# Kernel tuning notes

Hardware: AMD Instinct MI355X
Metric: run time of the kernel (lower is better)

## Reference

```python
import jax, jax.numpy as jnp
import numpy as np

B, S = 16, 256                     # batch, seq_len
CB, DB = 8, 256                    # control_bits, data_bits
IN_DIM = CB + DB                   # 264
OUT = DB                           # output_bits defaults to data_bits
H = 512                            # hidden_state_dim (LSTM controller)
M = 64                             # memory_content_size
R = 4                              # read heads
N = S                              # memory_addresses_size = -1 -> seq_len
_SPLITS = [R * M, R, M, 1, M, M, R, 1, 1, 3 * R]
XI = int(np.sum(_SPLITS))          # interface vector size = 471
_OFF = np.cumsum(_SPLITS)


def setup_inputs():
    ks = jax.random.split(jax.random.key(0), 6)
    sc = lambda k, shape: jax.random.normal(k, shape, jnp.float32) * 0.02
    return {
        "inputs": jax.random.normal(ks[0], (B, S, IN_DIM), jnp.float32),
        "Wx": sc(ks[1], (IN_DIM + R * M, 4 * H)),
        "Wh": sc(ks[2], (H, 4 * H)),
        "b_lstm": jnp.zeros((4 * H,), jnp.float32),
        "W_xi": sc(ks[3], (H, XI)),
        "b_xi": jnp.zeros((XI,), jnp.float32),
        "W_y": sc(ks[4], (H, OUT)),
        "W_r": sc(ks[5], (R * M, OUT)),
        "b_y": jnp.zeros((OUT,), jnp.float32),
    }


def _oneplus(x):
    return 1.0 + jax.nn.softplus(x)


def _content_weights(mem, keys, beta):
    # mem [B,N,M], keys [B,K,M], beta [B,K] -> softmax over N: [B,K,N]
    mem_n = mem / (jnp.linalg.norm(mem, axis=-1, keepdims=True) + 1e-6)
    key_n = keys / (jnp.linalg.norm(keys, axis=-1, keepdims=True) + 1e-6)
    sim = jnp.einsum('bkm,bnm->bkn', key_n, mem_n)
    return jax.nn.softmax(beta[..., None] * sim, axis=-1)


def _allocation(usage):
    # DNC paper allocation weighting via ascending usage sort
    idx = jnp.argsort(usage, axis=-1)
    u_s = jnp.take_along_axis(usage, idx, axis=-1)
    prod_excl = jnp.concatenate([jnp.ones_like(u_s[:, :1]), jnp.cumprod(u_s, axis=-1)[:, :-1]], axis=-1)
    a_s = (1.0 - u_s) * prod_excl
    inv = jnp.argsort(idx, axis=-1)
    return jnp.take_along_axis(a_s, inv, axis=-1)


def _dnc_forward(inputs, Wx, Wh, b_lstm, W_xi, b_xi, W_y, W_r_out, b_y):
    b = inputs.shape[0]
    eye = jnp.eye(N, dtype=inputs.dtype)

    def step(carry, x):
        h, c, mem, usage, link, prec, w_r, w_w, r_vec = carry
        # LSTM controller on [input, prev read vectors]
        ctrl_in = jnp.concatenate([x, r_vec.reshape(b, R * M)], axis=-1)
        gates = ctrl_in @ Wx + h @ Wh + b_lstm
        i_g, f_g, g_g, o_g = jnp.split(gates, 4, axis=-1)
        c = jax.nn.sigmoid(f_g) * c + jax.nn.sigmoid(i_g) * jnp.tanh(g_g)
        h = jax.nn.sigmoid(o_g) * jnp.tanh(c)

        # interface vector split
        xi = h @ W_xi + b_xi
        k_r = xi[:, :_OFF[0]].reshape(b, R, M)
        beta_r = _oneplus(xi[:, _OFF[0]:_OFF[1]])
        k_w = xi[:, _OFF[1]:_OFF[2]][:, None, :]
        beta_w = _oneplus(xi[:, _OFF[2]:_OFF[3]])
        erase = jax.nn.sigmoid(xi[:, _OFF[3]:_OFF[4]])
        w_vec = xi[:, _OFF[4]:_OFF[5]]
        free = jax.nn.sigmoid(xi[:, _OFF[5]:_OFF[6]])
        g_a = jax.nn.sigmoid(xi[:, _OFF[6]:_OFF[7]])
        g_w = jax.nn.sigmoid(xi[:, _OFF[7]:_OFF[8]])
        pi = jax.nn.softmax(xi[:, _OFF[8]:_OFF[9]].reshape(b, R, 3), axis=-1)

        # usage / allocation (content-free addressing)
        psi = jnp.prod(1.0 - free[:, :, None] * w_r, axis=1)           # [B,N]
        usage = (usage + w_w - usage * w_w) * psi
        alloc = _allocation(usage)

        # write weighting + memory scatter update
        c_w = _content_weights(mem, k_w, beta_w)[:, 0]                 # [B,N]
        w_w = g_w * (g_a * alloc + (1.0 - g_a) * c_w)
        mem = mem * (1.0 - w_w[:, :, None] * erase[:, None, :]) + w_w[:, :, None] * w_vec[:, None, :]

        # temporal linkage
        link = (1.0 - w_w[:, :, None] - w_w[:, None, :]) * link + w_w[:, :, None] * prec[:, None, :]
        link = link * (1.0 - eye)
        prec = (1.0 - jnp.sum(w_w, axis=-1, keepdims=True)) * prec + w_w

        # read weightings (backward / content / forward modes)
        fwd_w = jnp.einsum('bij,brj->bri', link, w_r)
        bwd_w = jnp.einsum('bji,brj->bri', link, w_r)
        c_r = _content_weights(mem, k_r, beta_r)                       # [B,R,N]
        w_r = pi[..., 0:1] * bwd_w + pi[..., 1:2] * c_r + pi[..., 2:3] * fwd_w
        r_vec = jnp.einsum('brn,bnm->brm', w_r, mem)                   # [B,R,M]

        y = h @ W_y + r_vec.reshape(b, R * M) @ W_r_out + b_y
        return (h, c, mem, usage, link, prec, w_r, w_w, r_vec), y

    z = jnp.zeros
    carry0 = (z((b, H)), z((b, H)), z((b, N, M)), z((b, N)), z((b, N, N)),
              z((b, N)), z((b, R, N)), z((b, N)), z((b, R, M)))
    _, ys = jax.lax.scan(step, carry0, jnp.swapaxes(inputs, 0, 1))
    return jnp.swapaxes(ys, 0, 1)                                      # [B,S,OUT]


def reference(inputs, Wx, Wh, b_lstm, W_xi, b_xi, W_y, W_r, b_y):
    return _dnc_forward(inputs, Wx, Wh, b_lstm, W_xi, b_xi, W_y, W_r, b_y)
```

## Files before the change

### kernel.cpp

```cpp
#include <hip/hip_runtime.h>
#include <cstddef>

#define DEV __device__ __forceinline__

constexpr int S_ = 256;
constexpr int NB = 256;
constexpr int NT = 256;


constexpr size_t bH    = 0;
constexpr size_t bC    = 1024;
constexpr size_t bXI   = 1536;
constexpr size_t bKNR  = 2048;
constexpr size_t bALC  = 2304;
constexpr size_t bCW   = 2560;
constexpr size_t bWW   = 2816;
constexpr size_t bNRM  = 3072;
constexpr size_t bUSG  = 3328;
constexpr size_t bRV   = 3584;
constexpr size_t bYH   = 3840;
constexpr size_t bSCL  = 4096;
constexpr size_t bPI   = 4128;
constexpr size_t bERS  = 4160;
constexpr size_t bWVC  = 4224;
constexpr size_t bPRC  = 4288;
constexpr size_t bWR   = 4800;
constexpr size_t bFWD  = 5824;
constexpr size_t bBWDP = 6848;
constexpr size_t bFLG  = 10944;
constexpr size_t bMEM  = 11456;
constexpr size_t bLNK  = 27840;
constexpr size_t bGT   = 93376;
constexpr size_t bGCT  = 95424;
constexpr size_t bSTF  = 95456;
constexpr size_t PB    = 95488;
constexpr size_t WS_TOTAL = PB*16;

typedef unsigned long long u64_;
union F2U { u64_ u; float2 f; };
DEV float2 ld2_agt(const float* p){ F2U c; c.u=__hip_atomic_load((const u64_*)p,__ATOMIC_RELAXED,__HIP_MEMORY_SCOPE_AGENT); return c.f; }
DEV void   st2_agt(float* p, float2 v){ F2U c; c.f=v; __hip_atomic_store((u64_*)p,c.u,__ATOMIC_RELAXED,__HIP_MEMORY_SCOPE_AGENT); }
DEV float  ld_agt(const float* p){ return __hip_atomic_load((float*)p,__ATOMIC_RELAXED,__HIP_MEMORY_SCOPE_AGENT); }
DEV void   st_agt(float* p,float v){ __hip_atomic_store(p,v,__ATOMIC_RELAXED,__HIP_MEMORY_SCOPE_AGENT); }
DEV float  ld_sys(const float* p){ return __hip_atomic_load((float*)p,__ATOMIC_RELAXED,__HIP_MEMORY_SCOPE_SYSTEM); }
DEV void   st_sys(float* p,float v){ __hip_atomic_store(p,v,__ATOMIC_RELAXED,__HIP_MEMORY_SCOPE_SYSTEM); }

DEV float sigm(float x){ return 1.0f/(1.0f+expf(-x)); }
DEV float oneplus_(float x){ float sp = (x>20.0f)? x : log1pf(expf(x)); return 1.0f+sp; }

DEV float wredsum(float v){
  #pragma unroll
  for (int o=32;o>0;o>>=1) v += __shfl_xor(v,o);
  return v;
}
DEV float hredsum32(float v){
  #pragma unroll
  for (int o=16;o>0;o>>=1) v += __shfl_xor(v,o);
  return v;
}
DEV float wredmax(float v){
  #pragma unroll
  for (int o=32;o>0;o>>=1) v = fmaxf(v,__shfl_xor(v,o));
  return v;
}
DEV float bredsum(float v, float* red){
  v = wredsum(v);
  if ((threadIdx.x&63)==0) red[threadIdx.x>>6]=v;
  __syncthreads();
  float r = red[0]+red[1]+red[2]+red[3];
  __syncthreads();
  return r;
}
DEV float bredmax(float v, float* red){
  v = wredmax(v);
  if ((threadIdx.x&63)==0) red[threadIdx.x>>6]=v;
  __syncthreads();
  float r = fmaxf(fmaxf(red[0],red[1]),fmaxf(red[2],red[3]));
  __syncthreads();
  return r;
}

DEV void cbar(float* wsb, unsigned ep, int ci){
  unsigned* flg = (unsigned*)(wsb + bFLG);
  __syncthreads();
  if (threadIdx.x < 64){
    if (threadIdx.x == 0)
      __hip_atomic_store(flg + (size_t)ci*32, ep, __ATOMIC_RELAXED, __HIP_MEMORY_SCOPE_AGENT);
    const int l = threadIdx.x;
    bool ok;
    do {
      unsigned v = (l<16) ? __hip_atomic_load(flg + (size_t)l*32,
                      __ATOMIC_RELAXED, __HIP_MEMORY_SCOPE_AGENT) : ep;
      ok = __all(v >= ep);
      if (!ok) __builtin_amdgcn_s_sleep(1);
    } while (!ok);
  }
  __syncthreads();
}

__global__ void k_zero(float* __restrict__ ws){
  size_t i = (size_t)blockIdx.x*blockDim.x + threadIdx.x;
  size_t st = (size_t)gridDim.x*blockDim.x;
  for (; i<WS_TOTAL; i+=st) ws[i]=0.0f;
}

__global__ __launch_bounds__(NT, 2) void k_dnc(
    const float* __restrict__ xin, const float* __restrict__ Wx,
    const float* __restrict__ Wh,  const float* __restrict__ bl,
    const float* __restrict__ Wxi, const float* __restrict__ bxi,
    const float* __restrict__ Wy,  const float* __restrict__ Wr,
    const float* __restrict__ by,  float* __restrict__ out,
    float* __restrict__ ws)
{
  __shared__ float smem[14336];
  const int tid  = threadIdx.x;
  const int bid  = blockIdx.x;
  const int lane = tid & 63, wv = tid >> 6;
  const int x  = bid & 7;
  const int q  = bid >> 3;
  const int s  = q & 1;
  const int ci = q >> 1;
  const int b  = x + (s<<3);
  float* wsb = ws + (size_t)b*PB;
  const int gb = ci;
  const int gh = s;
  float* wsg = ws + (size_t)gb*PB;
  unsigned ep = 0;

  for (int t=0; t<S_; ++t){
    {
      unsigned* stf = (unsigned*)(wsg + bSTF);
      if (tid==0){
        while (__hip_atomic_load(stf, __ATOMIC_RELAXED, __HIP_MEMORY_SCOPE_SYSTEM) < (unsigned)t)
          __builtin_amdgcn_s_sleep(1);
      }
      __syncthreads();
      float* sact = smem;
      float* sred = smem + 1040;
      const float* hrd = wsg + bH + (size_t)(t&1)*512;
      for (int e=tid; e<1032; e+=NT){
        float v;
        if (e < 264)      v = xin[((size_t)(gb*256+t))*264 + e];
        else if (e < 520) v = ld_sys(wsg + bRV + (e-264));
        else              v = ld_sys(hrd + (e-520));
        sact[e] = v;
      }
      __syncthreads();
      const int ks = tid>>5, c = tid&31;
      for (int j=0;j<4;++j){
        int g   = x + ((gh*4 + j)<<3);
        int col = (g<<5) + c;
        float a = 0.f;
        {
          const float* wp = Wx + (size_t)(ks*65)*2048 + col;
          const float* xp = sact + ks*65;
          #pragma unroll 8
          for (int k=0;k<65;++k) a = fmaf(xp[k], wp[(size_t)k*2048], a);
        }
        {
          const float* wp = Wh + (size_t)(ks*64)*2048 + col;
          const float* xp = sact + 520 + ks*64;
          #pragma unroll 8
          for (int k=0;k<64;++k) a = fmaf(xp[k], wp[(size_t)k*2048], a);
        }
        sred[ks*32 + c] = a;
        __syncthreads();
        if (tid < 32){
          float sm = bl[(g<<5) + tid];
          #pragma unroll
          for (int p=0;p<8;++p) sm += sred[p*32 + tid];
          st_sys(wsg + bGT + (g<<5) + tid, sm);
        }
        __syncthreads();
      }
      if (tid==0) atomicAdd((unsigned*)(wsg + bGCT), 1u);
    }

    {
      float* srv  = smem;
      float* ysum = smem + 256;
      if (t > 0){
        for (int e=tid;e<256;e+=NT) srv[e]=ld_sys(wsb+bRV+e);
        __syncthreads();
        int ks2 = tid>>4, cc = tid&15;
        int yc = (ci<<4) + cc;
        float a = 0.f;
        const float* wp = Wr + (size_t)(ks2*16)*256 + yc;
        const float* rp = srv + ks2*16;
        #pragma unroll
        for (int k=0;k<16;++k) a = fmaf(rp[k], wp[(size_t)k*256], a);
        ysum[ks2*16 + cc] = a;
        __syncthreads();
        if (tid < 16){
          float sm = 0.f;
          #pragma unroll
          for (int p=0;p<16;++p) sm += ysum[p*16 + tid];
          int yc2 = (ci<<4) + tid;
          out[((size_t)(b*256 + (t-1)))*256 + yc2] = ld_agt(wsb+bYH+yc2) + sm;
        }
        __syncthreads();
      }
      unsigned* gct = (unsigned*)(wsb + bGCT);
      if (tid==0){
        while (__hip_atomic_load(gct, __ATOMIC_RELAXED, __HIP_MEMORY_SCOPE_SYSTEM) < 16u*(unsigned)(t+1))
          __builtin_amdgcn_s_sleep(1);
      }
      __syncthreads();
      if (tid < 32){
        int j = (ci<<5) + tid;
        float gi = ld_sys(wsb+bGT+j);
        float gf = ld_sys(wsb+bGT+512+j);
        float gg2= ld_sys(wsb+bGT+1024+j);
        float go = ld_sys(wsb+bGT+1536+j);
        float co = wsb[bC + j];
        float cn = sigm(gf)*co + sigm(gi)*tanhf(gg2);
        float hn = sigm(go)*tanhf(cn);
        wsb[bC + j] = cn;
        st_sys(wsb + bH + (size_t)((t+1)&1)*512 + j, hn);
      }
    }
    ep++; cbar(wsb, ep, ci);

    {
      float* shh = smem;
      float* sp  = smem + 512;
      float* syh = smem + 768;
      const float* hcur = wsb + bH + (size_t)((t+1)&1)*512;
      for (int e=tid; e<512; e+=NT) shh[e] = ld_sys(hcur + e);
      __syncthreads();
      const int nc = (ci<15) ? 30 : 21;
      if (tid < 240){
        int ks = tid/30, cc = tid%30;
        if (cc < nc){
          int col = ci*30 + cc;
          float a = 0.f;
          const float* wp = Wxi + (size_t)(ks*64)*471 + col;
          const float* hp = shh + ks*64;
          #pragma unroll 8
          for (int k=0;k<64;++k) a = fmaf(hp[k], wp[(size_t)k*471], a);
          sp[ks*30 + cc] = a;
        }
      }
      {
        int ks = tid>>4, cc = tid&15;
        int col = (ci<<4) + cc;
        float a = 0.f;
        const float* wp = Wy + (size_t)(ks*32)*256 + col;
        const float* hp = shh + ks*32;
        #pragma unroll 8
        for (int k=0;k<32;++k) a = fmaf(hp[k], wp[(size_t)k*256], a);
        syh[ks*16 + cc] = a;
      }
      __syncthreads();
      if (tid < nc){
        float sm = bxi[ci*30 + tid];
        #pragma unroll
        for (int p=0;p<8;++p) sm += sp[p*30 + tid];
        st_agt(wsb + bXI + ci*30 + tid, sm);
      }
      if (tid < 16){
        float sm = by[(ci<<4) + tid];
        #pragma unroll
        for (int p=0;p<16;++p) sm += syh[p*16 + tid];
        st_agt(wsb + bYH + (ci<<4) + tid, sm);
      }
    }
    ep++; cbar(wsb, ep, ci);

    if (ci == 0){
      float* xv = smem; float* uu = smem+512; float* sa = smem+768;
      float* sb = smem+1024; float* red = smem+1280;
      if (tid < 240){
        float2 v = ld2_agt(wsb + bXI + (tid<<1));
        xv[tid<<1]=v.x; xv[(tid<<1)+1]=v.y;
      }
      __syncthreads();
      int n = tid;
      float f0=sigm(xv[453]), f1=sigm(xv[454]), f2v=sigm(xv[455]), f3=sigm(xv[456]);
      const float* wrb = wsb + bWR;
      float psi=(1.f-f0*ld_agt(wrb+n))*(1.f-f1*ld_agt(wrb+256+n))
               *(1.f-f2v*ld_agt(wrb+512+n))*(1.f-f3*ld_agt(wrb+768+n));
      float uo=wsb[bUSG+n];
      float wwp=ld_agt(wsb+bWW+n);
      float un=(uo+wwp-uo*wwp)*psi;
      uu[n]=un; wsb[bUSG+n]=un;
      __syncthreads();
      int rk=0;
      #pragma unroll 8
      for (int j=0;j<256;++j){
        float uj=uu[j];
        rk += (uj<un)||(uj==un && j<n);
      }
      sa[rk]=un;
      __syncthreads();
      float* cur=sa; float* nxt=sb;
      for (int off=1;off<256;off<<=1){
        float v=cur[n]; if (n>=off) v*=cur[n-off];
        nxt[n]=v;
        __syncthreads();
        float* tmp=cur; cur=nxt; nxt=tmp;
      }
      float pe = rk ? cur[rk-1] : 1.f;
      float al = (1.f-un)*pe;
      st_agt(wsb+bALC+n, al);
      float sumA = bredsum(al, red);
      if (tid==0){
        st_agt(wsb+bSCL+0, sigm(xv[457]));
        st_agt(wsb+bSCL+1, sigm(xv[458]));
        st_agt(wsb+bSCL+2, sumA);
      }
      {
        int r=tid>>6, m=tid&63;
        float kv=xv[(r<<6)+m];
        float s2=wredsum(kv*kv);
        float br=oneplus_(xv[256+r]);
        st_agt(wsb+bKNR+tid, kv*br/(sqrtf(s2)+1e-6f));
      }
      if (tid<4){
        float p0=xv[459+tid*3], p1=xv[460+tid*3], p2=xv[461+tid*3];
        float mx=fmaxf(p0,fmaxf(p1,p2));
        float e0=expf(p0-mx), e1=expf(p1-mx), e2=expf(p2-mx);
        float sm=e0+e1+e2;
        st_agt(wsb+bPI+tid*3+0, e0/sm);
        st_agt(wsb+bPI+tid*3+1, e1/sm);
        st_agt(wsb+bPI+tid*3+2, e2/sm);
      }
      if (tid<64){
        st_agt(wsb+bERS+tid, sigm(xv[325+tid]));
        st_agt(wsb+bWVC+tid, xv[389+tid]);
      }
    } else if (ci == 1){
      float* knw=smem; float* sims=smem+64; float* red=smem+320;
      const int half = lane>>5, l32 = lane&31;
      if (wv==0){
        float kv=ld_agt(wsb+bXI+260+lane);
        float s2=wredsum(kv*kv);
        float bw_=oneplus_(ld_agt(wsb+bXI+324));
        knw[lane]=kv*bw_/(sqrtf(s2)+1e-6f);
      }
      __syncthreads();
      const float* memb=wsb+bMEM;
      for (int i2=0;i2<32;++i2){
        int n=(wv<<6)+(i2<<1)+half;
        float2 v=ld2_agt(memb+(n<<6)+(l32<<1));
        float d=hredsum32(v.x*knw[l32<<1]+v.y*knw[(l32<<1)+1]);
        if (l32==0) sims[n]=d/(sqrtf(ld_agt(wsb+bNRM+n))+1e-6f);
      }
      __syncthreads();
      float sv=sims[tid];
      float mx=bredmax(sv,red); float e=expf(sv-mx); float sm=bredsum(e,red);
      st_agt(wsb+bCW+tid, e/sm);
    } else if (ci == 2){
      for (int e=tid;e<4096;e+=NT) st_agt(wsb+bBWDP+e, 0.f);
    }
    ep++; cbar(wsb, ep, ci);

    {
      float* wwl   = smem;
      float* wrl   = smem + 256;
      float* fpart = smem + 320;
      float* sscl  = smem + 576;
      const int ri = ci<<4;
      if (tid < 3) sscl[tid] = ld_agt(wsb+bSCL+tid);
      __syncthreads();
      float ga = sscl[0], gw = sscl[1], sA = sscl[2];
      float sww = gw*(ga*sA + (1.f-ga));
      int j = tid;
      float wj = gw*(ga*ld_agt(wsb+bALC+j) + (1.f-ga)*ld_agt(wsb+bCW+j));
      wwl[j] = wj;
      if (ci == 1) st_agt(wsb+bWW+j, wj);
      float pj = ld_agt(wsb+bPRC + (size_t)(t&1)*256 + j);
      if (ci == 0) st_agt(wsb+bPRC + (size_t)((t+1)&1)*256 + j, (1.f-sww)*pj + wj);
      const float* wrb = wsb + bWR;
      float wr0=ld_agt(wrb+j), wr1=ld_agt(wrb+256+j),
            wr2=ld_agt(wrb+512+j), wr3=ld_agt(wrb+768+j);
      if (tid < 64) wrl[(tid>>4)*16 + (tid&15)] = ld_agt(wrb + ((size_t)(tid>>4)<<8) + ri + (tid&15));
      __syncthreads();
      float b0=0.f,b1=0.f,b2=0.f,b3=0.f;
      float* lrow = wsb + bLNK + (size_t)ri*256;
      for (int il=0; il<16; ++il){
        int irow = ri + il;
        float Lo = lrow[il*256 + j];
        float wi = wwl[irow];
        float Ln = (1.f - wi - wj)*Lo + wi*pj;
        if (irow == j) Ln = 0.f;
        lrow[il*256 + j] = Ln;
        float s0=wredsum(Ln*wr0), s1=wredsum(Ln*wr1), s2=wredsum(Ln*wr2), s3=wredsum(Ln*wr3);
        if (lane==0){
          fpart[wv*64 + il]      = s0;
          fpart[wv*64 + 16 + il] = s1;
          fpart[wv*64 + 32 + il] = s2;
          fpart[wv*64 + 48 + il] = s3;
        }
        b0=fmaf(Ln, wrl[il],    b0);
        b1=fmaf(Ln, wrl[16+il], b1);
        b2=fmaf(Ln, wrl[32+il], b2);
        b3=fmaf(Ln, wrl[48+il], b3);
      }
      __syncthreads();
      if (tid < 64){
        int r = tid>>4, il = tid&15;
        float sm = fpart[r*16+il] + fpart[64+r*16+il] + fpart[128+r*16+il] + fpart[192+r*16+il];
        st_agt(wsb+bFWD + ((size_t)r<<8) + ri + il, sm);
      }
      float* slot = wsb + bBWDP + (size_t)(ci&3)*1024;
      atomicAdd(&slot[j], b0);      atomicAdd(&slot[256+j], b1);
      atomicAdd(&slot[512+j], b2);  atomicAdd(&slot[768+j], b3);
      {
        int row2 = tid>>5, c2 = tid&31;
        float2 er  = ld2_agt(wsb+bERS + (c2<<1));
        float2 wv2 = ld2_agt(wsb+bWVC + (c2<<1));
        #pragma unroll
        for (int it=0; it<2; ++it){
          int row = ri + row2 + it*8;
          float wwn = wwl[row];
          float2 v = ld2_agt(wsb+bMEM + ((size_t)row<<6) + (c2<<1));
          v.x = v.x*(1.f - wwn*er.x) + wwn*wv2.x;
          v.y = v.y*(1.f - wwn*er.y) + wwn*wv2.y;
          st2_agt(wsb+bMEM + ((size_t)row<<6) + (c2<<1), v);
          float s2 = hredsum32(v.x*v.x + v.y*v.y);
          if (c2==0) st_agt(wsb+bNRM+row, s2);
        }
      }
    }
    ep++; cbar(wsb, ep, ci);

    if (ci < 4){
      int r = ci;
      float* knl=smem; float* sims=smem+64; float* wrs=smem+320;
      float* part=smem+576; float* red=smem+832;
      if (wv==0) knl[lane]=ld_agt(wsb+bKNR+(r<<6)+lane);
      __syncthreads();
      const float* memb = wsb + bMEM;
      {
        int row2 = tid>>5, c2 = tid&31;
        for (int it=0; it<32; ++it){
          int n = row2 + it*8;
          float2 v = ld2_agt(memb + ((size_t)n<<6) + (c2<<1));
          float d = hredsum32(v.x*knl[c2<<1] + v.y*knl[(c2<<1)+1]);
          if (c2==0) sims[n] = d/(sqrtf(ld_agt(wsb+bNRM+n))+1e-6f);
        }
      }
      __syncthreads();
      float sv=sims[tid];
      float mx=bredmax(sv,red); float e=expf(sv-mx); float sm=bredsum(e,red);
      float cr=e/sm;
      float p0=ld_agt(wsb+bPI+r*3), p1=ld_agt(wsb+bPI+r*3+1), p2=ld_agt(wsb+bPI+r*3+2);
      float bwv = ld_agt(wsb+bBWDP + ((size_t)r<<8) + tid)
                + ld_agt(wsb+bBWDP + 1024 + ((size_t)r<<8) + tid)
                + ld_agt(wsb+bBWDP + 2048 + ((size_t)r<<8) + tid)
                + ld_agt(wsb+bBWDP + 3072 + ((size_t)r<<8) + tid);
      float wr = p0*bwv + p1*cr + p2*ld_agt(wsb+bFWD+((size_t)r<<8)+tid);
      st_agt(wsb+bWR+((size_t)r<<8)+tid, wr);
      wrs[tid]=wr;
      __syncthreads();
      {
        int m = tid&63, ksn = tid>>6;
        float a=0.f;
        #pragma unroll 8
        for (int n0=0;n0<64;++n0){
          int n = (ksn<<6)+n0;
          a = fmaf(wrs[n], ld_agt(memb + ((size_t)n<<6) + m), a);
        }
        part[(ksn<<6)+m]=a;
      }
      __syncthreads();
      if (tid<64)
        st_sys(wsb+bRV+(r<<6)+tid, part[tid]+part[64+tid]+part[128+tid]+part[192+tid]);
    }
    ep++; cbar(wsb, ep, ci);

    if (ci==0 && tid==0)
      __hip_atomic_store((unsigned*)(wsb + bSTF), (unsigned)(t+1),
                         __ATOMIC_RELAXED, __HIP_MEMORY_SCOPE_SYSTEM);
  }

  {
    float* srv  = smem;
    float* ysum = smem + 256;
    for (int e=tid;e<256;e+=NT) srv[e]=ld_sys(wsb+bRV+e);
    __syncthreads();
    int ks2 = tid>>4, cc = tid&15;
    int yc = (ci<<4) + cc;
    float a = 0.f;
    const float* wp = Wr + (size_t)(ks2*16)*256 + yc;
    const float* rp = srv + ks2*16;
    #pragma unroll
    for (int k=0;k<16;++k) a = fmaf(rp[k], wp[(size_t)k*256], a);
    ysum[ks2*16 + cc] = a;
    __syncthreads();
    if (tid < 16){
      float sm = 0.f;
      #pragma unroll
      for (int p=0;p<16;++p) sm += ysum[p*16 + tid];
      int yc2 = (ci<<4) + tid;
      out[((size_t)(b*256 + 255))*256 + yc2] = ld_agt(wsb+bYH+yc2) + sm;
    }
  }
}

extern "C" void kernel_launch(void* const* d_in, const int* in_sizes, int n_in,
                              void* d_out, int out_size, void* d_ws, size_t ws_size,
                              hipStream_t stream) {
  (void)in_sizes; (void)out_size;
  if (n_in < 9) return;
  const float* xin = (const float*)d_in[0];
  const float* Wx  = (const float*)d_in[1];
  const float* Wh  = (const float*)d_in[2];
  const float* bl  = (const float*)d_in[3];
  const float* Wxi = (const float*)d_in[4];
  const float* bxi = (const float*)d_in[5];
  const float* Wy  = (const float*)d_in[6];
  const float* Wr  = (const float*)d_in[7];
  const float* by  = (const float*)d_in[8];
  float* out = (float*)d_out;
  float* ws  = (float*)d_ws;
  if (ws_size < WS_TOTAL*sizeof(float)) return;

  hipLaunchKernelGGL(k_zero, dim3(512), dim3(256), 0, stream, ws);
  hipLaunchKernelGGL(k_dnc, dim3(NB), dim3(NT), 0, stream,
                     xin, Wx, Wh, bl, Wxi, bxi, Wy, Wr, by, out, ws);
}
```

Measured before the change: 25.18 ms.

## Fuse LSTM cell update into gate GEMV and drop a cluster barrier

Each block now computes all four gates (i,f,g,o) for the same 32 hidden units, splitting the K dimension between Wx and Wh across two halves of the block. This lets the block apply the LSTM cell update locally instead of writing gate pre-activations to global memory for another block to read. The per-step cluster barrier and the gate-count flag are replaced by a single h-count flag, and weight loads are software-prefetched in chunks of 16. The aim is to remove one global synchronisation and a round trip through memory per timestep. In exchange, each thread runs a longer serial reduction of about 520 terms, and the column mapping is reworked so each block's gate columns line up with its own hidden indices.

```diff
diff --git a/kernel.cpp b/kernel.cpp
--- a/kernel.cpp
+++ b/kernel.cpp
@@ -30,10 +30,9 @@
 constexpr size_t bFLG  = 10944;
 constexpr size_t bMEM  = 11456;
 constexpr size_t bLNK  = 27840;
-constexpr size_t bGT   = 93376;
-constexpr size_t bGCT  = 95424;
-constexpr size_t bSTF  = 95456;
-constexpr size_t PB    = 95488;
+constexpr size_t bHCT  = 93376;
+constexpr size_t bSTF  = 93408;
+constexpr size_t PB    = 93440;
 constexpr size_t WS_TOTAL = PB*16;
 
 typedef unsigned long long u64_;
@@ -123,7 +122,6 @@
   const int b  = x + (s<<3);
   float* wsb = ws + (size_t)b*PB;
   const int gb = ci;
-  const int gh = s;
   float* wsg = ws + (size_t)gb*PB;
   unsigned ep = 0;
 
@@ -137,6 +135,7 @@
       __syncthreads();
       float* sact = smem;
       float* sred = smem + 1040;
+      float* g4   = smem + 1296;
       const float* hrd = wsg + bH + (size_t)(t&1)*512;
       for (int e=tid; e<1032; e+=NT){
         float v;
@@ -146,34 +145,58 @@
         sact[e] = v;
       }
       __syncthreads();
-      const int ks = tid>>5, c = tid&31;
-      for (int j=0;j<4;++j){
-        int g   = x + ((gh*4 + j)<<3);
-        int col = (g<<5) + c;
-        float a = 0.f;
-        {
-          const float* wp = Wx + (size_t)(ks*65)*2048 + col;
-          const float* xp = sact + ks*65;
-          #pragma unroll 8
-          for (int k=0;k<65;++k) a = fmaf(xp[k], wp[(size_t)k*2048], a);
-        }
-        {
-          const float* wp = Wh + (size_t)(ks*64)*2048 + col;
-          const float* xp = sact + 520 + ks*64;
-          #pragma unroll 8
-          for (int k=0;k<64;++k) a = fmaf(xp[k], wp[(size_t)k*2048], a);
-        }
-        sred[ks*32 + c] = a;
-        __syncthreads();
-        if (tid < 32){
-          float sm = bl[(g<<5) + tid];
+      {
+        const int ks2 = tid>>7, cc = tid&127;
+        const int Q = cc>>5, mm = (cc>>3)&3, r = cc&7;
+        const int col = (Q<<9) + (x<<3) + (((s<<2)+mm)<<6) + r;
+        const float* W; const float* xp; int kn;
+        if (ks2==0){ W = Wx + col; xp = sact;       kn = 520; }
+        else       { W = Wh + col; xp = sact + 520; kn = 512; }
+        float acc = 0.f;
+        float buf[16];
+        const int nch = (kn+15)>>4;
+        #pragma unroll
+        for (int i=0;i<16;++i){
+          int kk = (i<kn)? i : kn-1;
+          buf[i] = W[(size_t)kk*2048];
+        }
+        for (int c2=0; c2<nch; ++c2){
+          float nb[16];
+          int nb0 = (c2+1)<<4;
           #pragma unroll
-          for (int p=0;p<8;++p) sm += sred[p*32 + tid];
-          st_sys(wsg + bGT + (g<<5) + tid, sm);
-        }
-        __syncthreads();
-      }
-      if (tid==0) atomicAdd((unsigned*)(wsg + bGCT), 1u);
+          for (int i=0;i<16;++i){
+            int kk = nb0+i; kk = (kk<kn)? kk : kn-1;
+            nb[i] = W[(size_t)kk*2048];
+          }
+          int kb = c2<<4;
+          #pragma unroll
+          for (int i=0;i<16;++i){
+            float xv = (kb+i<kn)? xp[kb+i] : 0.f;
+            acc = fmaf(buf[i], xv, acc);
+          }
+          #pragma unroll
+          for (int i=0;i<16;++i) buf[i]=nb[i];
+        }
+        sred[tid] = acc;
+      }
+      __syncthreads();
+      if (tid < 128){
+        const int Q = tid>>5, mm = (tid>>3)&3, r = tid&7;
+        const int col = (Q<<9) + (x<<3) + (((s<<2)+mm)<<6) + r;
+        g4[tid] = sred[tid] + sred[128+tid] + bl[col];
+      }
+      __syncthreads();
+      if (tid < 32){
+        int j = (x<<3) + (((s<<2)+(tid>>3))<<6) + (tid&7);
+        float gi=g4[tid], gf=g4[32+tid], gg2=g4[64+tid], go=g4[96+tid];
+        float co = wsg[bC + j];
+        float cn = sigm(gf)*co + sigm(gi)*tanhf(gg2);
+        float hn = sigm(go)*tanhf(cn);
+        wsg[bC + j] = cn;
+        st_sys(wsg + bH + (size_t)((t+1)&1)*512 + j, hn);
+      }
+      __syncthreads();
+      if (tid==0) atomicAdd((unsigned*)(wsg + bHCT), 1u);
     }
 
     {
@@ -200,28 +223,12 @@
         }
         __syncthreads();
       }
-      unsigned* gct = (unsigned*)(wsb + bGCT);
+      unsigned* hct = (unsigned*)(wsb + bHCT);
       if (tid==0){
-        while (__hip_atomic_load(gct, __ATOMIC_RELAXED, __HIP_MEMORY_SCOPE_SYSTEM) < 16u*(unsigned)(t+1))
+        while (__hip_atomic_load(hct, __ATOMIC_RELAXED, __HIP_MEMORY_SCOPE_SYSTEM) < 16u*(unsigned)(t+1))
           __builtin_amdgcn_s_sleep(1);
       }
       __syncthreads();
-      if (tid < 32){
-        int j = (ci<<5) + tid;
-        float gi = ld_sys(wsb+bGT+j);
-        float gf = ld_sys(wsb+bGT+512+j);
-        float gg2= ld_sys(wsb+bGT+1024+j);
-        float go = ld_sys(wsb+bGT+1536+j);
-        float co = wsb[bC + j];
-        float cn = sigm(gf)*co + sigm(gi)*tanhf(gg2);
-        float hn = sigm(go)*tanhf(cn);
-        wsb[bC + j] = cn;
-        st_sys(wsb + bH + (size_t)((t+1)&1)*512 + j, hn);
-      }
-    }
-    ep++; cbar(wsb, ep, ci);
-
-    {
       float* shh = smem;
       float* sp  = smem + 512;
       float* syh = smem + 768;
```

Measured after the change: 25.49 ms. No clear change (+1.2%).
